# Performance work log

Measured on AMD Instinct MI355X. Metric: run time of the kernel, lower is better.

Reference implementation:

```python
import jax, jax.numpy as jnp
import numpy as np

B, C, H, W = 8, 128, 64, 64


def setup_inputs() -> dict:
    key = jax.random.key(0)
    ks = jax.random.split(key, 8)
    s = 1.0 / np.sqrt(C)
    return {
        "x1": jax.random.normal(ks[0], (B, C, H, W), dtype=jnp.float32),
        "x2": jax.random.normal(ks[1], (B, C, H, W), dtype=jnp.float32),
        "Wq": jax.random.normal(ks[2], (C, C), dtype=jnp.float32) * s,
        "bq": jax.random.normal(ks[3], (C,), dtype=jnp.float32) * s,
        "Wk": jax.random.normal(ks[4], (C, C), dtype=jnp.float32) * s,
        "bk": jax.random.normal(ks[5], (C,), dtype=jnp.float32) * s,
        "Wv": jax.random.normal(ks[6], (C, C), dtype=jnp.float32) * s,
        "bv": jax.random.normal(ks[7], (C,), dtype=jnp.float32) * s,
    }


def reference(x1, x2, Wq, bq, Wk, bk, Wv, bv):
    b, c, h, w = x1.shape
    n = h * w
    # 1x1 conv == channel matmul per pixel; flatten spatial dims -> [b, c, n]
    x1f = x1.reshape(b, c, n)
    x2f = x2.reshape(b, c, n)
    q = jnp.einsum("oc,bcn->bno", Wq, x1f) + bq[None, None, :]  # [b, n, c]
    k = jnp.einsum("oc,bcn->bon", Wk, x2f) + bk[None, :, None]  # [b, c, n]
    v = jnp.einsum("oc,bcn->bon", Wv, x2f) + bv[None, :, None]  # [b, c, n]
    energy = jnp.einsum("bnc,bcm->bnm", q, k)                   # [b, n, n] (unscaled)
    attention = jax.nn.softmax(energy, axis=-1)
    # out[b,c,i] = sum_j v[b,c,j] * attention[b,i,j]
    out = jnp.einsum("bcj,bij->bci", v, attention)
    return out.reshape(b, c, h, w)
```

## Files before the change

### kernel.cpp

```cpp
#include <hip/hip_runtime.h>

typedef float f4 __attribute__((ext_vector_type(4)));
typedef float f16v __attribute__((ext_vector_type(16)));
typedef _Float16 hf;
typedef __fp16 fp16x2 __attribute__((ext_vector_type(2)));
typedef hf h8 __attribute__((ext_vector_type(8)));
typedef unsigned short ushort_t;
typedef unsigned int uint_t;
typedef uint_t u4 __attribute__((ext_vector_type(4)));

#define BATCH 8
#define CH 128
#define NPIX 4096
#define LOG2E 1.4426950408889634f
#define RESCALE_THR 8.0f

__device__ inline f16v mfma32h(h8 a, h8 b, f16v c) {
    return __builtin_amdgcn_mfma_f32_32x32x16_f16(a, b, c, 0, 0, 0);
}

__device__ inline uint_t pk2h(float a, float b) {
    fp16x2 pp = __builtin_amdgcn_cvt_pkrtz(a, b);
    union { fp16x2 v; uint_t u; } cv;
    cv.v = pp;
    return cv.u;
}

__device__ inline void pl32swap(uint_t& a, uint_t& b) {
    asm("v_permlane32_swap_b32 %0, %1" : "+v"(a), "+v"(b));
}

typedef __attribute__((address_space(3))) uint_t lds_uint;
typedef __attribute__((address_space(1))) const uint_t global_uint;
__device__ inline void dma16(const void* g, void* l) {
    __builtin_amdgcn_global_load_lds((global_uint*)g, (lds_uint*)l, 16, 0, 0);
}

__device__ inline ushort_t h2u(hf x) {
    union { hf h; ushort_t u; } cv;
    cv.h = x;
    return cv.u;
}

__global__ __launch_bounds__(256) void qkv_kernel(const float* __restrict__ x1,
                                                  const float* __restrict__ x2,
                                                  const float* __restrict__ Wq,
                                                  const float* __restrict__ Wk,
                                                  const float* __restrict__ Wv,
                                                  const float* __restrict__ bq,
                                                  const float* __restrict__ bk,
                                                  const float* __restrict__ bv,
                                                  hf* __restrict__ Qf, hf* __restrict__ Kf,
                                                  hf* __restrict__ Vf) {
    __shared__ __align__(16) ushort_t XH[64 * 128];
    __shared__ __align__(16) ushort_t XL[64 * 128];

    int bid = blockIdx.x;
    int m = bid >> 9;
    int rem = bid & 511;
    int b = rem & 7;
    int n0 = (rem >> 3) << 6;

    const float* X = ((m == 0) ? x1 : x2) + (size_t)b * CH * NPIX;
    const float* bias = (m == 0) ? bq : (m == 1) ? bk : bv;

    int tid = threadIdx.x;
#pragma unroll
    for (int r = 0; r < 8; ++r) {
        int c = 16 * r + (tid >> 4);
        int n4 = (tid & 15) << 2;
        f4 v = *(const f4*)&X[(size_t)c * NPIX + n0 + n4];
        int cs = c >> 3, cj = c & 7;
#pragma unroll
        for (int j = 0; j < 4; ++j) {
            int n = n4 + j;
            hf hi = (hf)v[j];
            hf lo = (hf)(v[j] - (float)hi);
            int ofs = n * 128 + ((cs ^ (n & 15)) << 3) + cj;
            XH[ofs] = h2u(hi);
            XL[ofs] = h2u(lo);
        }
    }

    int lane = tid & 63;
    int w = tid >> 6;
    int h = lane >> 5;
    int m32 = lane & 31;
    int o0 = w * 32;

    const float* Wsrc = (m == 0) ? Wq : (m == 1) ? Wk : Wv;
    float wscale = (m == 0) ? LOG2E : 1.0f;
    h8 wf[8];
    {
        const float* wrow = Wsrc + (size_t)(o0 + m32) * CH;
#pragma unroll
        for (int kc = 0; kc < 8; ++kc) {
            f4 a = *(const f4*)&wrow[kc * 16 + h * 8];
            f4 b2 = *(const f4*)&wrow[kc * 16 + h * 8 + 4];
            h8 t;
#pragma unroll
            for (int j = 0; j < 4; ++j) {
                t[j] = (hf)(a[j] * wscale);
                t[4 + j] = (hf)(b2[j] * wscale);
            }
            wf[kc] = t;
        }
    }

    __syncthreads();

    f16v acc[2];
#pragma unroll
    for (int g = 0; g < 2; ++g)
#pragma unroll
        for (int r = 0; r < 16; ++r) acc[g][r] = 0.f;

    int swzn = m32 & 15;
#pragma unroll
    for (int g = 0; g < 2; ++g) {
        int nrow = (g * 32 + m32) * 128;
#pragma unroll
        for (int kc = 0; kc < 8; ++kc) {
            int sofs = nrow + (((kc * 2 + h) ^ swzn) << 3);
            h8 xh = *(const h8*)&XH[sofs];
            h8 xl = *(const h8*)&XL[sofs];
            if (m == 2) {
                acc[g] = mfma32h(wf[kc], xh, acc[g]);
                acc[g] = mfma32h(wf[kc], xl, acc[g]);
            } else {
                acc[g] = mfma32h(xh, wf[kc], acc[g]);
                acc[g] = mfma32h(xl, wf[kc], acc[g]);
            }
        }
    }

    if (m < 2) {
        float bval = bias[o0 + m32] * ((m == 0) ? LOG2E : 1.0f);
        hf* Y = ((m == 0) ? Qf : Kf) + (size_t)b * NPIX * CH;
#pragma unroll
        for (int g = 0; g < 2; ++g)
#pragma unroll
            for (int r = 0; r < 16; ++r) {
                int n = n0 + g * 32 + (r & 3) + 8 * (r >> 2) + 4 * h;
                Y[(size_t)n * CH + o0 + m32] = (hf)(acc[g][r] + bval);
            }
    } else {
        hf* Yv = Vf + (size_t)b * CH * NPIX;
#pragma unroll
        for (int g = 0; g < 2; ++g)
#pragma unroll
            for (int r = 0; r < 16; ++r) {
                int o = o0 + (r & 3) + 8 * (r >> 2) + 4 * h;
                Yv[(size_t)o * NPIX + n0 + g * 32 + m32] = (hf)(acc[g][r] + bias[o]);
            }
    }
}

__global__ __launch_bounds__(256, 3) void attn_kernel(const hf* __restrict__ Qf,
                                                      const hf* __restrict__ Kf,
                                                      const hf* __restrict__ Vf,
                                                      hf* __restrict__ Opart,
                                                      float* __restrict__ Mpart,
                                                      float* __restrict__ Lpart) {
    __shared__ __align__(16) ushort_t smem[16384];

    int tid = threadIdx.x;
    int lane = tid & 63;
    int w = tid >> 6;
    int h = lane >> 5;
    int m32 = lane & 31;

    int idx = blockIdx.x;
    int b = idx & 7;
    int ks = (idx >> 3) & 3;
    int qt = idx >> 5;
    int q0 = (qt << 7) + w * 32;
    int k0g = ks << 10;

    const hf* Qb = Qf + (size_t)b * NPIX * CH;
    const hf* Kb = Kf + (size_t)b * NPIX * CH;
    const hf* Vb = Vf + (size_t)b * CH * NPIX;

    h8 qf[8];
#pragma unroll
    for (int kc = 0; kc < 8; ++kc)
        qf[kc] = *(const h8*)&Qb[(size_t)(q0 + m32) * CH + kc * 16 + h * 8];

    const hf* pK[2];
    const hf* pV[2];
#pragma unroll
    for (int a = 0; a < 2; ++a) {
        int chunk_hi = w * 2 + a;
        int rowk = chunk_hi * 4 + (lane >> 4);
        int lck = (lane & 15) ^ (rowk & 15);
        pK[a] = Kb + (size_t)(k0g + rowk) * CH + lck * 8;
        int rowv = chunk_hi * 16 + (lane >> 2);
        int lcv = (lane & 3) ^ (rowv & 3) ^ ((rowv >> 2) & 1);
        pV[a] = Vb + (size_t)rowv * NPIX + k0g + lcv * 8;
    }

#pragma unroll
    for (int a = 0; a < 2; ++a) {
        dma16(pK[a], &smem[(w * 2 + a) * 512]);
        dma16(pV[a], &smem[8192 + (w * 2 + a) * 512]);
        pK[a] += 32 * CH;
        pV[a] += 32;
    }

    f16v accO[4];
#pragma unroll
    for (int ct = 0; ct < 4; ++ct)
#pragma unroll
        for (int r = 0; r < 16; ++r) accO[ct][r] = 0.f;
    float mprev = -1e30f;
    float lsum = 0.f;

    int pvs[2];
#pragma unroll
    for (int g2 = 0; g2 < 2; ++g2)
        pvs[g2] = (g2 * 2 + h) ^ (m32 & 3) ^ ((m32 >> 2) & 1);

    __syncthreads();

    for (int t = 0; t < 32; ++t) {
        int cur = t & 1;
        if (t < 31) {
            int nb = 1 - cur;
#pragma unroll
            for (int a = 0; a < 2; ++a) {
                dma16(pK[a], &smem[nb * 4096 + (w * 2 + a) * 512]);
                dma16(pV[a], &smem[8192 + nb * 4096 + (w * 2 + a) * 512]);
                pK[a] += 32 * CH;
                pV[a] += 32;
            }
        }
        const ushort_t* kb = smem + cur * 4096;
        const ushort_t* vb = smem + 8192 + cur * 4096;

        f16v acc;
#pragma unroll
        for (int r = 0; r < 16; ++r) acc[r] = 0.f;
        __builtin_amdgcn_s_setprio(1);
#pragma unroll
        for (int kc = 0; kc < 8; ++kc) {
            int pA = (kc * 2 + h) ^ (m32 & 15);
            h8 ahi = *(const h8*)&kb[m32 * 128 + pA * 8];
            acc = mfma32h(ahi, qf[kc], acc);
        }
        __builtin_amdgcn_s_setprio(0);

        float ta = fmaxf(fmaxf(acc[0], acc[1]), acc[2]);
        float tb = fmaxf(fmaxf(acc[3], acc[4]), acc[5]);
        ta = fmaxf(fmaxf(ta, acc[6]), acc[7]);
        tb = fmaxf(fmaxf(tb, acc[8]), acc[9]);
        ta = fmaxf(fmaxf(ta, acc[10]), acc[11]);
        tb = fmaxf(fmaxf(tb, acc[12]), acc[13]);
        ta = fmaxf(fmaxf(ta, acc[14]), acc[15]);
        float tmax = fmaxf(ta, tb);
        tmax = fmaxf(tmax, __shfl_xor(tmax, 32));
        if (__any(tmax > mprev + RESCALE_THR)) {
            float mnew = fmaxf(mprev, tmax);
            float alpha = exp2f(mprev - mnew);
            lsum *= alpha;
#pragma unroll
            for (int ct = 0; ct < 4; ++ct)
#pragma unroll
                for (int r = 0; r < 16; ++r) accO[ct][r] *= alpha;
            mprev = mnew;
        }

        uint_t pk[8];
        float ps0 = 0.f, ps1 = 0.f;
#pragma unroll
        for (int t2 = 0; t2 < 8; ++t2) {
            float e0 = exp2f(acc[2 * t2] - mprev);
            float e1 = exp2f(acc[2 * t2 + 1] - mprev);
            ps0 += e0;
            ps1 += e1;
            pk[t2] = pk2h(e0, e1);
        }
        float psum = ps0 + ps1;
        psum += __shfl_xor(psum, 32);
        lsum += psum;

        pl32swap(pk[0], pk[2]);
        pl32swap(pk[1], pk[3]);
        pl32swap(pk[4], pk[6]);
        pl32swap(pk[5], pk[7]);
        h8 pbp[2];
#pragma unroll
        for (int g2 = 0; g2 < 2; ++g2) {
            u4 fv;
            fv[0] = pk[g2 * 4 + 0];
            fv[1] = pk[g2 * 4 + 1];
            fv[2] = pk[g2 * 4 + 2];
            fv[3] = pk[g2 * 4 + 3];
            __builtin_memcpy(&pbp[g2], &fv, 16);
        }

        __builtin_amdgcn_s_setprio(1);
#pragma unroll
        for (int g2 = 0; g2 < 2; ++g2) {
            int pv = pvs[g2];
#pragma unroll
            for (int ct = 0; ct < 4; ++ct) {
                h8 av = *(const h8*)&vb[(ct * 32 + m32) * 32 + pv * 8];
                accO[ct] = mfma32h(av, pbp[g2], accO[ct]);
            }
        }
        __builtin_amdgcn_s_setprio(0);

        __syncthreads();
    }

    size_t base = (((size_t)ks * 8 + b) * 32 + qt) * 16384;
    size_t mlb = (((size_t)ks * 8 + b) * 32 + qt) * 128;
    int q = w * 32 + m32;
#pragma unroll
    for (int ct = 0; ct < 4; ++ct)
#pragma unroll
        for (int r = 0; r < 16; ++r) {
            int ch = ct * 32 + (r & 3) + 8 * (r >> 2) + 4 * h;
            Opart[base + ch * 128 + q] = (hf)accO[ct][r];
        }
    if (h == 0) {
        Mpart[mlb + q] = mprev;
        Lpart[mlb + q] = lsum;
    }
}

__global__ __launch_bounds__(256) void combine_kernel(const hf* __restrict__ Opart,
                                                      const float* __restrict__ Mp,
                                                      const float* __restrict__ Lp,
                                                      float* __restrict__ out) {
    int idx = blockIdx.x;
    int chh = idx & 1;
    int b = (idx >> 1) & 7;
    int qt = idx >> 4;
    int tid = threadIdx.x;
    int q8 = (tid & 15) << 3;
    int chl = tid >> 4;

    size_t tile = (size_t)b * 32 + qt;

    float Marr[4][8], Larr[4][8];
#pragma unroll
    for (int p = 0; p < 4; ++p) {
        const float* mp_ = Mp + ((size_t)p * 256 + tile) * 128 + q8;
        const float* lp_ = Lp + ((size_t)p * 256 + tile) * 128 + q8;
        f4 ma = *(const f4*)mp_;
        f4 mb = *(const f4*)(mp_ + 4);
        f4 la = *(const f4*)lp_;
        f4 lb = *(const f4*)(lp_ + 4);
#pragma unroll
        for (int j = 0; j < 4; ++j) {
            Marr[p][j] = ma[j];
            Marr[p][4 + j] = mb[j];
            Larr[p][j] = la[j];
            Larr[p][4 + j] = lb[j];
        }
    }

    float wgt[4][8];
#pragma unroll
    for (int j = 0; j < 8; ++j) {
        float M = fmaxf(fmaxf(Marr[0][j], Marr[1][j]), fmaxf(Marr[2][j], Marr[3][j]));
        float L = 0.f;
#pragma unroll
        for (int p = 0; p < 4; ++p) {
            float w_ = exp2f(Marr[p][j] - M);
            wgt[p][j] = w_;
            L += w_ * Larr[p][j];
        }
        float rd = 1.0f / L;
#pragma unroll
        for (int p = 0; p < 4; ++p) wgt[p][j] *= rd;
    }

    const hf* ob[4];
#pragma unroll
    for (int p = 0; p < 4; ++p) ob[p] = Opart + ((size_t)p * 256 + tile) * 16384 + q8;
    float* O = out + (size_t)b * CH * NPIX + (size_t)qt * 128 + q8;

#pragma unroll
    for (int it = 0; it < 4; ++it) {
        int ch = chh * 64 + it * 16 + chl;
        union { u4 u; h8 v; } o4[4];
#pragma unroll
        for (int p = 0; p < 4; ++p) o4[p].u = *(const u4*)&ob[p][(size_t)ch * 128];
        f4 r0, r1;
#pragma unroll
        for (int j = 0; j < 8; ++j) {
            float s = 0.f;
#pragma unroll
            for (int p = 0; p < 4; ++p) s += wgt[p][j] * (float)o4[p].v[j];
            if (j < 4) r0[j] = s;
            else r1[j - 4] = s;
        }
        float* dst = O + (size_t)ch * NPIX;
        *(f4*)dst = r0;
        *(f4*)(dst + 4) = r1;
    }
}

extern "C" void kernel_launch(void* const* d_in, const int* in_sizes, int n_in,
                              void* d_out, int out_size, void* d_ws, size_t ws_size,
                              hipStream_t stream) {
    const float* x1 = (const float*)d_in[0];
    const float* x2 = (const float*)d_in[1];
    const float* Wq = (const float*)d_in[2];
    const float* bq = (const float*)d_in[3];
    const float* Wk = (const float*)d_in[4];
    const float* bk = (const float*)d_in[5];
    const float* Wv = (const float*)d_in[6];
    const float* bv = (const float*)d_in[7];
    float* outp = (float*)d_out;

    const size_t N = (size_t)BATCH * NPIX * CH;
    hf* Qf = (hf*)d_ws;
    hf* Kf = Qf + N;
    hf* Vf = Qf + 2 * N;
    hf* Opart = Qf + 3 * N;
    float* Mp = (float*)(Opart + (size_t)4 * 8 * 32 * 16384);
    float* Lp = Mp + (size_t)4 * 8 * 32 * 128;

    qkv_kernel<<<3 * BATCH * (NPIX / 64), 256, 0, stream>>>(x1, x2, Wq, Wk, Wv,
                                                            bq, bk, bv, Qf, Kf, Vf);
    attn_kernel<<<BATCH * 4 * (NPIX / 128), 256, 0, stream>>>(Qf, Kf, Vf, Opart, Mp, Lp);
    combine_kernel<<<2 * BATCH * (NPIX / 128), 256, 0, stream>>>(Opart, Mp, Lp, outp);
}
```

Baseline: 210.7 us.

## Triple-buffer K/V tiles with a single barrier per iteration and deferred lsum shuffle

Grows the shared K/V staging from two buffers to three and prefetches two tiles ahead. Each iteration now does one explicit vmcnt wait plus one barrier at the top instead of a trailing __syncthreads, which gives loads more time in flight and removes a synchronization point. The per-iteration cross-half shuffles for the row max and partial sum are also removed. The max shuffle now runs only inside the rescale branch, and the sum is reduced once after the loop. The larger LDS footprint (48 KB) may reduce how many blocks fit per CU, and the hand-written waitcnt depends on the exact count of outstanding DMA ops.

Result: no change. 209.9 us (-0.3%).

```diff
diff --git a/kernel.cpp b/kernel.cpp
--- a/kernel.cpp
+++ b/kernel.cpp
@@ -162,7 +162,7 @@
                                                       hf* __restrict__ Opart,
                                                       float* __restrict__ Mpart,
                                                       float* __restrict__ Lpart) {
-    __shared__ __align__(16) ushort_t smem[16384];
+    __shared__ __align__(16) ushort_t smem[24576];
 
     int tid = threadIdx.x;
     int lane = tid & 63;
@@ -200,11 +200,14 @@
     }
 
 #pragma unroll
-    for (int a = 0; a < 2; ++a) {
-        dma16(pK[a], &smem[(w * 2 + a) * 512]);
-        dma16(pV[a], &smem[8192 + (w * 2 + a) * 512]);
-        pK[a] += 32 * CH;
-        pV[a] += 32;
+    for (int tp = 0; tp < 2; ++tp) {
+#pragma unroll
+        for (int a = 0; a < 2; ++a) {
+            dma16(pK[a], &smem[tp * 4096 + (w * 2 + a) * 512]);
+            dma16(pV[a], &smem[12288 + tp * 4096 + (w * 2 + a) * 512]);
+            pK[a] += 32 * CH;
+            pV[a] += 32;
+        }
     }
 
     f16v accO[4];
@@ -220,22 +223,24 @@
     for (int g2 = 0; g2 < 2; ++g2)
         pvs[g2] = (g2 * 2 + h) ^ (m32 & 3) ^ ((m32 >> 2) & 1);
 
-    __syncthreads();
-
+    int br = 0, bw = 2;
     for (int t = 0; t < 32; ++t) {
-        int cur = t & 1;
-        if (t < 31) {
-            int nb = 1 - cur;
+        if (t < 31) asm volatile("s_waitcnt vmcnt(4) lgkmcnt(0)" ::: "memory");
+        else        asm volatile("s_waitcnt vmcnt(0) lgkmcnt(0)" ::: "memory");
+        __builtin_amdgcn_s_barrier();
+        __builtin_amdgcn_sched_barrier(0);
+
+        if (t < 30) {
 #pragma unroll
             for (int a = 0; a < 2; ++a) {
-                dma16(pK[a], &smem[nb * 4096 + (w * 2 + a) * 512]);
-                dma16(pV[a], &smem[8192 + nb * 4096 + (w * 2 + a) * 512]);
+                dma16(pK[a], &smem[bw * 4096 + (w * 2 + a) * 512]);
+                dma16(pV[a], &smem[12288 + bw * 4096 + (w * 2 + a) * 512]);
                 pK[a] += 32 * CH;
                 pV[a] += 32;
             }
         }
-        const ushort_t* kb = smem + cur * 4096;
-        const ushort_t* vb = smem + 8192 + cur * 4096;
+        const ushort_t* kb = smem + br * 4096;
+        const ushort_t* vb = smem + 12288 + br * 4096;
 
         f16v acc;
 #pragma unroll
@@ -257,9 +262,9 @@
         tb = fmaxf(fmaxf(tb, acc[12]), acc[13]);
         ta = fmaxf(fmaxf(ta, acc[14]), acc[15]);
         float tmax = fmaxf(ta, tb);
-        tmax = fmaxf(tmax, __shfl_xor(tmax, 32));
         if (__any(tmax > mprev + RESCALE_THR)) {
-            float mnew = fmaxf(mprev, tmax);
+            float tx = fmaxf(tmax, __shfl_xor(tmax, 32));
+            float mnew = fmaxf(mprev, tx);
             float alpha = exp2f(mprev - mnew);
             lsum *= alpha;
 #pragma unroll
@@ -279,9 +284,7 @@
             ps1 += e1;
             pk[t2] = pk2h(e0, e1);
         }
-        float psum = ps0 + ps1;
-        psum += __shfl_xor(psum, 32);
-        lsum += psum;
+        lsum += ps0 + ps1;
 
         pl32swap(pk[0], pk[2]);
         pl32swap(pk[1], pk[3]);
@@ -310,8 +313,11 @@
         }
         __builtin_amdgcn_s_setprio(0);
 
-        __syncthreads();
-    }
+        br = (br == 2) ? 0 : br + 1;
+        bw = (bw == 2) ? 0 : bw + 1;
+    }
+
+    lsum += __shfl_xor(lsum, 32);
 
     size_t base = (((size_t)ks * 8 + b) * 32 + qt) * 16384;
     size_t mlb = (((size_t)ks * 8 + b) * 32 + qt) * 128;
```
